# Kernel optimization log

Hardware: AMD Instinct MI355X
Metric: run time of the kernel (lower is better)

The kernel has to match this reference:

```python
import jax, jax.numpy as jnp
import numpy as np

N = 20000      # nodes
DEG = 16       # neighbors per destination node
E = N * DEG    # edges
G = 16         # graphs in batch


def _glorot(k, shape):
    lim = float(np.sqrt(6.0 / (shape[0] + shape[1])))
    return jax.random.uniform(k, shape, jnp.float32, -lim, lim)


def setup_inputs() -> dict:
    key = jax.random.key(0)
    ks = jax.random.split(key, 16)
    pos = jax.random.normal(ks[0], (N, 3), jnp.float32)
    edge_src = jax.random.randint(ks[1], (E,), 0, N)               # random neighbors
    edge_dst = jnp.repeat(jnp.arange(N), DEG)                       # every node is a dst
    batch = (jnp.arange(N) * G) // N                                # 16 contiguous graphs
    inp = {
        "pos": pos, "edge_src": edge_src, "edge_dst": edge_dst, "batch": batch,
        # conv1: mlp Linear(3+3 -> 128), Linear(128 -> 128)
        "c1_W1": _glorot(ks[2], (6, 128)),   "c1_b1": jnp.zeros((128,), jnp.float32),
        "c1_W2": _glorot(ks[3], (128, 128)), "c1_b2": jnp.zeros((128,), jnp.float32),
        # conv2: mlp Linear(128+3 -> 256), Linear(256 -> 256)
        "c2_W1": _glorot(ks[4], (131, 256)), "c2_b1": jnp.zeros((256,), jnp.float32),
        "c2_W2": _glorot(ks[5], (256, 256)), "c2_b2": jnp.zeros((256,), jnp.float32),
        "fc1_W": _glorot(ks[6], (256, 256)), "fc1_b": jnp.zeros((256,), jnp.float32),
        "fc2_W": _glorot(ks[7], (256, 128)), "fc2_b": jnp.zeros((128,), jnp.float32),
        "lab_W": _glorot(ks[8], (128, 10)),  "lab_b": jnp.zeros((10,), jnp.float32),
        "box_W": _glorot(ks[9], (128, 6)),   "box_b": jnp.zeros((6,), jnp.float32),
    }
    return inp


def _pointnet_conv(x, pos, src, dst, W1, b1, W2, b2):
    # gather: x_j, pos_j - pos_i per edge
    rel = pos[src] - pos[dst]                          # [E, 3]
    msg = jnp.concatenate([x[src], rel], axis=-1)      # [E, Cin+3]
    h = jnp.maximum(msg @ W1 + b1, 0.0) @ W2 + b2      # [E, Cout]
    # scatter-max aggregation per destination node (all nodes covered)
    return jax.ops.segment_max(h, dst, num_segments=N)


def reference(pos, edge_src, edge_dst, batch,
              c1_W1, c1_b1, c1_W2, c1_b2,
              c2_W1, c2_b1, c2_W2, c2_b2,
              fc1_W, fc1_b, fc2_W, fc2_b,
              lab_W, lab_b, box_W, box_b):
    x = pos  # model uses data.pos as both x and pos
    x = _pointnet_conv(x, pos, edge_src, edge_dst, c1_W1, c1_b1, c1_W2, c1_b2)
    x = _pointnet_conv(x, pos, edge_src, edge_dst, c2_W1, c2_b1, c2_W2, c2_b2)
    x = jax.ops.segment_max(x, batch, num_segments=G)  # global_max_pool -> [G, 256]
    x = jnp.maximum(x @ fc1_W + fc1_b, 0.0)
    x = jnp.maximum(x @ fc2_W + fc2_b, 0.0)
    labels = x @ lab_W + lab_b                          # [G, 10]
    bbox = x @ box_W + box_b                            # [G, 6]
    return (labels, bbox)
```

## Files before the change

kernel.cpp:

```cpp
#include <hip/hip_runtime.h>

#define N_NODES 20000
#define DEG 16
#define GRAPHS 16
#define NPG 1250

typedef __bf16 bf16x8 __attribute__((ext_vector_type(8)));
typedef float f32x4 __attribute__((ext_vector_type(4)));
#define MFMA16(a, b, c) __builtin_amdgcn_mfma_f32_16x16x32_bf16(a, b, c, 0, 0, 0)

__device__ __forceinline__ void ldsbar() {
    __asm__ volatile("s_waitcnt lgkmcnt(0)\n\ts_barrier" ::: "memory");
}
__device__ __forceinline__ void async16(void* lds, const void* g) {
    __builtin_amdgcn_global_load_lds(
        (const __attribute__((address_space(1))) unsigned int*)(g),
        (__attribute__((address_space(3))) unsigned int*)(lds), 16, 0, 0);
}

#define OFF_X1    0
#define OFF_P1    2560000
#define OFF_P2    2564096
#define OFF_P3    2580480
#define OFF_P4    2621440
#define OFF_POOL_BYTES 5373952
#define OFF_RELE  2695176
#define RELZ_ROW  320000
#define OFF_H1_BYTES 10510400

__global__ __launch_bounds__(256) void pack_weights(
    const float* __restrict__ c1W1, const float* __restrict__ c1W2,
    const float* __restrict__ c2W1, const float* __restrict__ c2W2,
    __bf16* __restrict__ p1, __bf16* __restrict__ p2,
    __bf16* __restrict__ p3, __bf16* __restrict__ p4,
    unsigned int* __restrict__ pooled, __bf16* __restrict__ relE)
{
    int t = blockIdx.x * 256 + threadIdx.x;
    if (t < GRAPHS * 256) pooled[t] = 0u;
    if (t == 0) {
        bf16x8 z;
        #pragma unroll
        for (int j = 0; j < 8; j++) z[j] = (__bf16)0.f;
        *(bf16x8*)&relE[(size_t)RELZ_ROW * 8] = z;
    }
    if (t >= 15872) return;
    const float* W; __bf16* out; int M, Kreal, KT, grp;
    if      (t <  512)  { W = c1W1; out = p1; M = 128; Kreal =   6; KT = 1; grp = t; }
    else if (t < 2560)  { W = c1W2; out = p2; M = 128; Kreal = 128; KT = 4; grp = t - 512; }
    else if (t < 7680)  { W = c2W1; out = p3; M = 256; Kreal = 131; KT = 5; grp = t - 2560; }
    else                { W = c2W2; out = p4; M = 256; Kreal = 256; KT = 8; grp = t - 7680; }
    int lane = grp & 63, rest = grp >> 6;
    int kt = rest % KT, mt = rest / KT;
    int m = mt * 16 + (lane & 15);
    int kbase = kt * 32 + ((lane >> 4) << 3);
    bf16x8 v;
    #pragma unroll
    for (int j = 0; j < 8; j++) {
        int k = kbase + j;
        v[j] = (k < Kreal) ? (__bf16)W[k * M + m] : (__bf16)0.f;
    }
    *(bf16x8*)&out[grp * 8] = v;
}

#define NB1 16
__global__ __launch_bounds__(256, 2) void conv1_kernel(
    const float* __restrict__ pos, const int* __restrict__ esrc,
    const __bf16* __restrict__ W1p, const float* __restrict__ b1,
    const __bf16* __restrict__ W2p, const float* __restrict__ b2,
    __bf16* __restrict__ x1, __bf16* __restrict__ relE)
{
    __shared__ __attribute__((aligned(16))) __bf16 msgF[NB1][16][8];
    __shared__ __attribute__((aligned(16))) __bf16 hidF[NB1 * 4 * 64 * 8];
    const int tid = threadIdx.x, lane = tid & 63, wave = tid >> 6;
    const int quad = lane >> 4, col = lane & 15;
    const int node0 = blockIdx.x * NB1;

    bf16x8 A1[2], B2w[2][4];
    f32x4 bias1[2];
    float b2v[2];
    #pragma unroll
    for (int i = 0; i < 2; i++) {
        int mtg = wave * 2 + i;
        A1[i] = *(const bf16x8*)&W1p[(mtg * 64 + lane) * 8];
        bias1[i] = *(const f32x4*)&b1[mtg * 16 + quad * 4];
        #pragma unroll
        for (int kt = 0; kt < 4; kt++)
            B2w[i][kt] = *(const bf16x8*)&W2p[((mtg * 4 + kt) * 64 + lane) * 8];
        b2v[i] = b2[mtg * 16 + col];
    }

    {
        int nl = tid >> 4, e = tid & 15;
        int d = node0 + nl;
        int s = esrc[d * 16 + e];
        float sx = pos[3*s], sy = pos[3*s+1], sz = pos[3*s+2];
        float dx = pos[3*d], dy = pos[3*d+1], dz = pos[3*d+2];
        __bf16 rx = (__bf16)(sx - dx), ry = (__bf16)(sy - dy), rz = (__bf16)(sz - dz);
        bf16x8 v;
        v[0] = (__bf16)sx; v[1] = (__bf16)sy; v[2] = (__bf16)sz;
        v[3] = rx; v[4] = ry; v[5] = rz;
        v[6] = (__bf16)0.f; v[7] = (__bf16)0.f;
        *(bf16x8*)&msgF[nl][e][0] = v;
        bf16x8 rv;
        rv[0] = rx; rv[1] = ry; rv[2] = rz;
        #pragma unroll
        for (int j = 3; j < 8; j++) rv[j] = (__bf16)0.f;
        *(bf16x8*)&relE[((size_t)d * 16 + e) * 8] = rv;
    }
    ldsbar();

    #pragma unroll
    for (int nl = 0; nl < NB1; nl++) {
        bf16x8 B;
        if (quad == 0) {
            B = *(const bf16x8*)&msgF[nl][col][0];
        } else {
            #pragma unroll
            for (int j = 0; j < 8; j++) B[j] = (__bf16)0.f;
        }
        #pragma unroll
        for (int i = 0; i < 2; i++) {
            int mtg = wave * 2 + i;
            f32x4 acc = bias1[i];
            acc = MFMA16(A1[i], B, acc);
            union { __bf16 h[4]; uint2 u; } pk;
            #pragma unroll
            for (int r = 0; r < 4; r++) pk.h[r] = (__bf16)fmaxf(acc[r], 0.f);
            int kt2 = mtg >> 1;
            int lane2 = ((mtg * 2 + (quad >> 1)) & 3) * 16 + col;
            int j0 = (quad & 1) * 4;
            *(uint2*)&hidF[((nl * 4 + kt2) * 64 + lane2) * 8 + j0] = pk.u;
        }
    }
    ldsbar();

    #pragma unroll
    for (int nl = 0; nl < NB1; nl++) {
        bf16x8 hA[4];
        #pragma unroll
        for (int kt = 0; kt < 4; kt++)
            hA[kt] = *(const bf16x8*)&hidF[((nl * 4 + kt) * 64 + lane) * 8];
        f32x4 acc[2];
        f32x4 z = {0.f, 0.f, 0.f, 0.f};
        acc[0] = z; acc[1] = z;
        #pragma unroll
        for (int kt = 0; kt < 4; kt++) {
            #pragma unroll
            for (int i = 0; i < 2; i++) acc[i] = MFMA16(hA[kt], B2w[i][kt], acc[i]);
        }
        #pragma unroll
        for (int i = 0; i < 2; i++) {
            int mtg = wave * 2 + i;
            float m = fmaxf(fmaxf(acc[i][0], acc[i][1]), fmaxf(acc[i][2], acc[i][3]));
            m = fmaxf(m, __shfl_xor(m, 16));
            m = fmaxf(m, __shfl_xor(m, 32));
            if (lane < 16)
                x1[(size_t)(node0 + nl) * 128 + mtg * 16 + lane] = (__bf16)(m + b2v[i]);
        }
    }
}

#define NB2 2
#define NT2 20
__global__ __launch_bounds__(512) __attribute__((amdgpu_waves_per_eu(2, 2)))
void conv2_kernel(
    const int* __restrict__ esrc,
    const __bf16* __restrict__ x1, const __bf16* __restrict__ relE,
    const __bf16* __restrict__ W1p, const float* __restrict__ b1,
    const __bf16* __restrict__ W2p, const float* __restrict__ b2,
    unsigned int* __restrict__ pooled)
{
    __shared__ __attribute__((aligned(16))) __bf16 msgF[3][NB2 * 5 * 64 * 8];
    __shared__ __attribute__((aligned(16))) __bf16 hidF[2][NB2 * 8 * 64 * 8];
    __shared__ int sSrc[NB2 * NT2 * 16];
    const int tid = threadIdx.x, lane = tid & 63, wave = tid >> 6;
    const int quad = lane >> 4, col = lane & 15;
    const int base = blockIdx.x * (NB2 * NT2);

    for (int u = tid; u < NB2 * NT2 * 16; u += 512) sSrc[u] = esrc[base * 16 + u];
    __syncthreads();

    if (wave < 4) {
        bf16x8 A1[4][5];
        f32x4 bias1[4];
        #pragma unroll
        for (int i = 0; i < 4; i++) {
            int tg = wave * 4 + i;
            #pragma unroll
            for (int kt = 0; kt < 5; kt++)
                A1[i][kt] = *(const bf16x8*)&W1p[((tg * 5 + kt) * 64 + lane) * 8];
            bias1[i] = *(const f32x4*)&b1[tg * 16 + quad * 4];
        }

        auto stage = [&](int td, int buf) {
            #pragma unroll
            for (int s = 0; s < 3; s++) {
                int g = wave + 4 * s;
                if (g < 10) {
                    int nl = g / 5, kt = g % 5;
                    __bf16* ldst = &msgF[buf][g * 64 * 8];
                    const __bf16* gsrc;
                    if (kt < 4) {
                        int src = sSrc[(td * NB2 + nl) * 16 + col];
                        gsrc = &x1[(size_t)src * 128 + kt * 32 + quad * 8];
                    } else {
                        int row = (quad == 0) ? ((base + td * NB2 + nl) * 16 + col) : RELZ_ROW;
                        gsrc = &relE[(size_t)row * 8];
                    }
                    async16(ldst, gsrc);
                }
            }
        };

        stage(0, 0);
        stage(1, 1);

        for (int k = 0; k < NT2; k++) {
            int td = k + 2;
            if (td >= NT2) td -= NT2;
            stage(td, (k + 2) % 3);
            if (wave < 2) __asm__ volatile("s_waitcnt vmcnt(6)" ::: "memory");
            else          __asm__ volatile("s_waitcnt vmcnt(4)" ::: "memory");
            const int bufi = k % 3, bufo = k & 1;
            #pragma unroll
            for (int nl = 0; nl < NB2; nl++) {
                bf16x8 B[5];
                #pragma unroll
                for (int kt = 0; kt < 5; kt++)
                    B[kt] = *(const bf16x8*)&msgF[bufi][((nl * 5 + kt) * 64 + lane) * 8];
                #pragma unroll
                for (int i = 0; i < 4; i++) {
                    int mtg = wave * 4 + i;
                    f32x4 acc = bias1[i];
                    #pragma unroll
                    for (int kt = 0; kt < 5; kt++) acc = MFMA16(A1[i][kt], B[kt], acc);
                    union { __bf16 h[4]; uint2 u; } pk;
                    #pragma unroll
                    for (int r = 0; r < 4; r++) pk.h[r] = (__bf16)fmaxf(acc[r], 0.f);
                    int kt2 = mtg >> 1;
                    int lane2 = ((mtg * 2 + (quad >> 1)) & 3) * 16 + col;
                    int j0 = (quad & 1) * 4;
                    *(uint2*)&hidF[bufo][((nl * 8 + kt2) * 64 + lane2) * 8 + j0] = pk.u;
                }
            }
            ldsbar();
        }
    } else {
        const int wv = wave - 4;
        bf16x8 B2r[4][8];
        #pragma unroll
        for (int i = 0; i < 4; i++) {
            int tg = wv * 4 + i;
            #pragma unroll
            for (int kt = 0; kt < 8; kt++)
                B2r[i][kt] = *(const bf16x8*)&W2p[((tg * 8 + kt) * 64 + lane) * 8];
        }
        f32x4 runmax[4];
        #pragma unroll
        for (int i = 0; i < 4; i++)
            #pragma unroll
            for (int r = 0; r < 4; r++) runmax[i][r] = -3.4e38f;
        int gprev = base / NPG;

        auto flushfn = [&]() {
            #pragma unroll
            for (int i = 0; i < 4; i++) {
                float v = fmaxf(fmaxf(runmax[i][0], runmax[i][1]),
                                fmaxf(runmax[i][2], runmax[i][3]));
                v = fmaxf(v, __shfl_xor(v, 16));
                v = fmaxf(v, __shfl_xor(v, 32));
                if (lane < 16) {
                    int c = (wv * 4 + i) * 16 + lane;
                    float val = v + b2[c];
                    unsigned u = __float_as_uint(val);
                    u = (u & 0x80000000u) ? ~u : (u | 0x80000000u);
                    atomicMax(&pooled[gprev * 256 + c], u);
                }
                #pragma unroll
                for (int r = 0; r < 4; r++) runmax[i][r] = -3.4e38f;
            }
        };
        auto consume = [&](int tk) {
            int buf1 = tk & 1;
            int n0 = base + tk * NB2;
            #pragma unroll
            for (int nl = 0; nl < NB2; nl++) {
                int g = (n0 + nl) / NPG;
                if (g != gprev) { flushfn(); gprev = g; }
                bf16x8 hA[8];
                #pragma unroll
                for (int kt = 0; kt < 8; kt++)
                    hA[kt] = *(const bf16x8*)&hidF[buf1][((nl * 8 + kt) * 64 + lane) * 8];
                f32x4 acc[4];
                f32x4 z = {0.f, 0.f, 0.f, 0.f};
                #pragma unroll
                for (int i = 0; i < 4; i++) acc[i] = z;
                #pragma unroll
                for (int kt = 0; kt < 8; kt++) {
                    #pragma unroll
                    for (int i = 0; i < 4; i++) acc[i] = MFMA16(hA[kt], B2r[i][kt], acc[i]);
                }
                #pragma unroll
                for (int i = 0; i < 4; i++)
                    #pragma unroll
                    for (int r = 0; r < 4; r++)
                        runmax[i][r] = fmaxf(runmax[i][r], acc[i][r]);
            }
        };

        for (int k = 0; k < NT2; k++) {
            ldsbar();
            consume(k);
        }
        flushfn();
    }
}

__global__ __launch_bounds__(256) void head1_kernel(
    const unsigned int* __restrict__ pooled,
    const float* __restrict__ fc1_W, const float* __restrict__ fc1_b,
    float* __restrict__ h1)
{
    __shared__ float p[256];
    const int g = blockIdx.x, c = threadIdx.x;
    unsigned u = pooled[g * 256 + c];
    u = (u & 0x80000000u) ? (u & 0x7fffffffu) : ~u;
    p[c] = __uint_as_float(u);
    __syncthreads();
    float acc = fc1_b[c];
    #pragma unroll 8
    for (int k = 0; k < 256; k++) acc += p[k] * fc1_W[k * 256 + c];
    h1[g * 256 + c] = fmaxf(acc, 0.f);
}

__global__ __launch_bounds__(128) void head2_kernel(
    const float* __restrict__ h1,
    const float* __restrict__ fc2_W, const float* __restrict__ fc2_b,
    const float* __restrict__ lab_W, const float* __restrict__ lab_b,
    const float* __restrict__ box_W, const float* __restrict__ box_b,
    float* __restrict__ out)
{
    __shared__ float hs[256];
    __shared__ float h2s[128];
    const int g = blockIdx.x, c = threadIdx.x;
    hs[c]       = h1[g * 256 + c];
    hs[c + 128] = h1[g * 256 + 128 + c];
    __syncthreads();
    float acc = fc2_b[c];
    #pragma unroll 8
    for (int k = 0; k < 256; k++) acc += hs[k] * fc2_W[k * 128 + c];
    h2s[c] = fmaxf(acc, 0.f);
    __syncthreads();
    if (c < 10) {
        float a = lab_b[c];
        #pragma unroll 8
        for (int k = 0; k < 128; k++) a += h2s[k] * lab_W[k * 10 + c];
        out[g * 10 + c] = a;
    } else if (c < 16) {
        int j = c - 10;
        float a = box_b[j];
        #pragma unroll 8
        for (int k = 0; k < 128; k++) a += h2s[k] * box_W[k * 6 + j];
        out[160 + g * 6 + j] = a;
    }
}

extern "C" void kernel_launch(void* const* d_in, const int* in_sizes, int n_in,
                              void* d_out, int out_size, void* d_ws, size_t ws_size,
                              hipStream_t stream) {
    const float* pos   = (const float*)d_in[0];
    const int*   esrc  = (const int*)  d_in[1];
    const float* c1W1 = (const float*)d_in[4];
    const float* c1b1 = (const float*)d_in[5];
    const float* c1W2 = (const float*)d_in[6];
    const float* c1b2 = (const float*)d_in[7];
    const float* c2W1 = (const float*)d_in[8];
    const float* c2b1 = (const float*)d_in[9];
    const float* c2W2 = (const float*)d_in[10];
    const float* c2b2 = (const float*)d_in[11];
    const float* fc1W = (const float*)d_in[12];
    const float* fc1b = (const float*)d_in[13];
    const float* fc2W = (const float*)d_in[14];
    const float* fc2b = (const float*)d_in[15];
    const float* labW = (const float*)d_in[16];
    const float* labb = (const float*)d_in[17];
    const float* boxW = (const float*)d_in[18];
    const float* boxb = (const float*)d_in[19];

    __bf16* wsb = (__bf16*)d_ws;
    __bf16* x1   = wsb + OFF_X1;
    __bf16* p1   = wsb + OFF_P1;
    __bf16* p2   = wsb + OFF_P2;
    __bf16* p3   = wsb + OFF_P3;
    __bf16* p4   = wsb + OFF_P4;
    __bf16* relE = wsb + OFF_RELE;
    unsigned int* pooled = (unsigned int*)((char*)d_ws + OFF_POOL_BYTES);
    float* h1 = (float*)((char*)d_ws + OFF_H1_BYTES);

    pack_weights<<<62, 256, 0, stream>>>(c1W1, c1W2, c2W1, c2W2, p1, p2, p3, p4, pooled, relE);
    conv1_kernel<<<N_NODES / NB1, 256, 0, stream>>>(pos, esrc, p1, c1b1, p2, c1b2, x1, relE);
    conv2_kernel<<<N_NODES / (NB2 * NT2), 512, 0, stream>>>(esrc, x1, relE, p3, c2b1, p4, c2b2, pooled);
    head1_kernel<<<GRAPHS, 256, 0, stream>>>(pooled, fc1W, fc1b, h1);
    head2_kernel<<<GRAPHS, 128, 0, stream>>>(h1, fc2W, fc2b, labW, labb, boxW, boxb, (float*)d_out);
}
```

Before: 215.6 us.

## Split edge gather into own kernel, warp-specialize conv1, fuse head kernels

Edge message construction (source position plus relative position) now runs in a separate gather kernel that writes a full 8-wide bf16 message per edge. Conv2's packed first-layer weights are remapped so its rel slot reads from columns 3-5 of that message. Conv1 becomes a producer/consumer kernel: four waves async-load messages into triple-buffered LDS and run layer 1, while four waves run layer 2 and the max reduction from double-buffered hidden tiles. The two head kernels are merged into one 1024-thread kernel with split-K reductions, which removes a launch and the h1 round trip. The cost is an extra launch and a global write and read of per-edge messages.

```diff
diff --git a/kernel.cpp b/kernel.cpp
--- a/kernel.cpp
+++ b/kernel.cpp
@@ -24,16 +24,15 @@
 #define OFF_P3    2580480
 #define OFF_P4    2621440
 #define OFF_POOL_BYTES 5373952
-#define OFF_RELE  2695176
-#define RELZ_ROW  320000
-#define OFF_H1_BYTES 10510400
+#define OFF_MSGE  2695176
+#define ZROW      320000
 
 __global__ __launch_bounds__(256) void pack_weights(
     const float* __restrict__ c1W1, const float* __restrict__ c1W2,
     const float* __restrict__ c2W1, const float* __restrict__ c2W2,
     __bf16* __restrict__ p1, __bf16* __restrict__ p2,
     __bf16* __restrict__ p3, __bf16* __restrict__ p4,
-    unsigned int* __restrict__ pooled, __bf16* __restrict__ relE)
+    unsigned int* __restrict__ pooled, __bf16* __restrict__ msgE)
 {
     int t = blockIdx.x * 256 + threadIdx.x;
     if (t < GRAPHS * 256) pooled[t] = 0u;
@@ -41,13 +40,13 @@
         bf16x8 z;
         #pragma unroll
         for (int j = 0; j < 8; j++) z[j] = (__bf16)0.f;
-        *(bf16x8*)&relE[(size_t)RELZ_ROW * 8] = z;
+        *(bf16x8*)&msgE[(size_t)ZROW * 8] = z;
     }
     if (t >= 15872) return;
-    const float* W; __bf16* out; int M, Kreal, KT, grp;
+    const float* W; __bf16* out; int M, Kreal, KT, grp; bool c2w1 = false;
     if      (t <  512)  { W = c1W1; out = p1; M = 128; Kreal =   6; KT = 1; grp = t; }
     else if (t < 2560)  { W = c1W2; out = p2; M = 128; Kreal = 128; KT = 4; grp = t - 512; }
-    else if (t < 7680)  { W = c2W1; out = p3; M = 256; Kreal = 131; KT = 5; grp = t - 2560; }
+    else if (t < 7680)  { W = c2W1; out = p3; M = 256; Kreal = 131; KT = 5; grp = t - 2560; c2w1 = true; }
     else                { W = c2W2; out = p4; M = 256; Kreal = 256; KT = 8; grp = t - 7680; }
     int lane = grp & 63, rest = grp >> 6;
     int kt = rest % KT, mt = rest / KT;
@@ -56,106 +55,125 @@
     bf16x8 v;
     #pragma unroll
     for (int j = 0; j < 8; j++) {
-        int k = kbase + j;
-        v[j] = (k < Kreal) ? (__bf16)W[k * M + m] : (__bf16)0.f;
+        int ks = kbase + j;
+        int wr;
+        if (c2w1) wr = (ks < 128) ? ks : ((ks >= 131 && ks < 134) ? ks - 3 : -1);
+        else      wr = (ks < Kreal) ? ks : -1;
+        v[j] = (wr >= 0) ? (__bf16)W[wr * M + m] : (__bf16)0.f;
     }
     *(bf16x8*)&out[grp * 8] = v;
 }
 
-#define NB1 16
-__global__ __launch_bounds__(256, 2) void conv1_kernel(
+__global__ __launch_bounds__(256) void gatherE_kernel(
     const float* __restrict__ pos, const int* __restrict__ esrc,
+    __bf16* __restrict__ msgE)
+{
+    int e = blockIdx.x * 256 + threadIdx.x;
+    int d = e >> 4;
+    int s = esrc[e];
+    float sx = pos[3*s], sy = pos[3*s+1], sz = pos[3*s+2];
+    float dx = pos[3*d], dy = pos[3*d+1], dz = pos[3*d+2];
+    bf16x8 v;
+    v[0] = (__bf16)sx; v[1] = (__bf16)sy; v[2] = (__bf16)sz;
+    v[3] = (__bf16)(sx - dx); v[4] = (__bf16)(sy - dy); v[5] = (__bf16)(sz - dz);
+    v[6] = (__bf16)0.f; v[7] = (__bf16)0.f;
+    *(bf16x8*)&msgE[(size_t)e * 8] = v;
+}
+
+#define NB1T 4
+#define NT1 10
+__global__ __launch_bounds__(512, 4) void conv1_kernel(
+    const __bf16* __restrict__ msgE,
     const __bf16* __restrict__ W1p, const float* __restrict__ b1,
     const __bf16* __restrict__ W2p, const float* __restrict__ b2,
-    __bf16* __restrict__ x1, __bf16* __restrict__ relE)
+    __bf16* __restrict__ x1)
 {
-    __shared__ __attribute__((aligned(16))) __bf16 msgF[NB1][16][8];
-    __shared__ __attribute__((aligned(16))) __bf16 hidF[NB1 * 4 * 64 * 8];
+    __shared__ __attribute__((aligned(16))) __bf16 msgF[3][NB1T * 64 * 8];
+    __shared__ __attribute__((aligned(16))) __bf16 hidF[2][NB1T * 4 * 64 * 8];
     const int tid = threadIdx.x, lane = tid & 63, wave = tid >> 6;
     const int quad = lane >> 4, col = lane & 15;
-    const int node0 = blockIdx.x * NB1;
-
-    bf16x8 A1[2], B2w[2][4];
-    f32x4 bias1[2];
-    float b2v[2];
-    #pragma unroll
-    for (int i = 0; i < 2; i++) {
-        int mtg = wave * 2 + i;
-        A1[i] = *(const bf16x8*)&W1p[(mtg * 64 + lane) * 8];
-        bias1[i] = *(const f32x4*)&b1[mtg * 16 + quad * 4];
-        #pragma unroll
-        for (int kt = 0; kt < 4; kt++)
-            B2w[i][kt] = *(const bf16x8*)&W2p[((mtg * 4 + kt) * 64 + lane) * 8];
-        b2v[i] = b2[mtg * 16 + col];
-    }
-
-    {
-        int nl = tid >> 4, e = tid & 15;
-        int d = node0 + nl;
-        int s = esrc[d * 16 + e];
-        float sx = pos[3*s], sy = pos[3*s+1], sz = pos[3*s+2];
-        float dx = pos[3*d], dy = pos[3*d+1], dz = pos[3*d+2];
-        __bf16 rx = (__bf16)(sx - dx), ry = (__bf16)(sy - dy), rz = (__bf16)(sz - dz);
-        bf16x8 v;
-        v[0] = (__bf16)sx; v[1] = (__bf16)sy; v[2] = (__bf16)sz;
-        v[3] = rx; v[4] = ry; v[5] = rz;
-        v[6] = (__bf16)0.f; v[7] = (__bf16)0.f;
-        *(bf16x8*)&msgF[nl][e][0] = v;
-        bf16x8 rv;
-        rv[0] = rx; rv[1] = ry; rv[2] = rz;
-        #pragma unroll
-        for (int j = 3; j < 8; j++) rv[j] = (__bf16)0.f;
-        *(bf16x8*)&relE[((size_t)d * 16 + e) * 8] = rv;
-    }
-    ldsbar();
-
-    #pragma unroll
-    for (int nl = 0; nl < NB1; nl++) {
-        bf16x8 B;
-        if (quad == 0) {
-            B = *(const bf16x8*)&msgF[nl][col][0];
-        } else {
-            #pragma unroll
-            for (int j = 0; j < 8; j++) B[j] = (__bf16)0.f;
-        }
+    const int base = blockIdx.x * (NB1T * NT1);
+
+    if (wave < 4) {
+        bf16x8 A1[2];
+        f32x4 bias1[2];
         #pragma unroll
         for (int i = 0; i < 2; i++) {
             int mtg = wave * 2 + i;
-            f32x4 acc = bias1[i];
-            acc = MFMA16(A1[i], B, acc);
-            union { __bf16 h[4]; uint2 u; } pk;
-            #pragma unroll
-            for (int r = 0; r < 4; r++) pk.h[r] = (__bf16)fmaxf(acc[r], 0.f);
-            int kt2 = mtg >> 1;
-            int lane2 = ((mtg * 2 + (quad >> 1)) & 3) * 16 + col;
-            int j0 = (quad & 1) * 4;
-            *(uint2*)&hidF[((nl * 4 + kt2) * 64 + lane2) * 8 + j0] = pk.u;
-        }
-    }
-    ldsbar();
-
-    #pragma unroll
-    for (int nl = 0; nl < NB1; nl++) {
-        bf16x8 hA[4];
-        #pragma unroll
-        for (int kt = 0; kt < 4; kt++)
-            hA[kt] = *(const bf16x8*)&hidF[((nl * 4 + kt) * 64 + lane) * 8];
-        f32x4 acc[2];
-        f32x4 z = {0.f, 0.f, 0.f, 0.f};
-        acc[0] = z; acc[1] = z;
-        #pragma unroll
-        for (int kt = 0; kt < 4; kt++) {
-            #pragma unroll
-            for (int i = 0; i < 2; i++) acc[i] = MFMA16(hA[kt], B2w[i][kt], acc[i]);
-        }
+            A1[i] = *(const bf16x8*)&W1p[(mtg * 64 + lane) * 8];
+            bias1[i] = *(const f32x4*)&b1[mtg * 16 + quad * 4];
+        }
+        auto stage = [&](int td, int buf) {
+            int nl = wave;
+            int row = (quad == 0) ? ((base + td * NB1T + nl) * 16 + col) : ZROW;
+            async16(&msgF[buf][nl * 64 * 8], &msgE[(size_t)row * 8]);
+        };
+        stage(0, 0);
+        stage(1, 1);
+        for (int k = 0; k < NT1; k++) {
+            int td = k + 2; if (td >= NT1) td -= NT1;
+            stage(td, (k + 2) % 3);
+            __asm__ volatile("s_waitcnt vmcnt(2)" ::: "memory");
+            const int bufi = k % 3, bufo = k & 1;
+            #pragma unroll
+            for (int nl = 0; nl < NB1T; nl++) {
+                bf16x8 B = *(const bf16x8*)&msgF[bufi][(nl * 64 + lane) * 8];
+                #pragma unroll
+                for (int i = 0; i < 2; i++) {
+                    int mtg = wave * 2 + i;
+                    f32x4 acc = bias1[i];
+                    acc = MFMA16(A1[i], B, acc);
+                    union { __bf16 h[4]; uint2 u; } pk;
+                    #pragma unroll
+                    for (int r = 0; r < 4; r++) pk.h[r] = (__bf16)fmaxf(acc[r], 0.f);
+                    int kt2 = mtg >> 1;
+                    int lane2 = ((mtg * 2 + (quad >> 1)) & 3) * 16 + col;
+                    int j0 = (quad & 1) * 4;
+                    *(uint2*)&hidF[bufo][((nl * 4 + kt2) * 64 + lane2) * 8 + j0] = pk.u;
+                }
+            }
+            ldsbar();
+        }
+    } else {
+        const int wv = wave - 4;
+        bf16x8 B2w[2][4];
+        float b2v[2];
         #pragma unroll
         for (int i = 0; i < 2; i++) {
-            int mtg = wave * 2 + i;
-            float m = fmaxf(fmaxf(acc[i][0], acc[i][1]), fmaxf(acc[i][2], acc[i][3]));
-            m = fmaxf(m, __shfl_xor(m, 16));
-            m = fmaxf(m, __shfl_xor(m, 32));
-            if (lane < 16)
-                x1[(size_t)(node0 + nl) * 128 + mtg * 16 + lane] = (__bf16)(m + b2v[i]);
+            int mtg = wv * 2 + i;
+            #pragma unroll
+            for (int kt = 0; kt < 4; kt++)
+                B2w[i][kt] = *(const bf16x8*)&W2p[((mtg * 4 + kt) * 64 + lane) * 8];
+            b2v[i] = b2[mtg * 16 + col];
+        }
+        for (int k = 0; k < NT1; k++) {
+            ldsbar();
+            const int buf = k & 1;
+            const int n0 = base + k * NB1T;
+            #pragma unroll
+            for (int nl = 0; nl < NB1T; nl++) {
+                bf16x8 hA[4];
+                #pragma unroll
+                for (int kt = 0; kt < 4; kt++)
+                    hA[kt] = *(const bf16x8*)&hidF[buf][((nl * 4 + kt) * 64 + lane) * 8];
+                f32x4 acc[2];
+                f32x4 z = {0.f, 0.f, 0.f, 0.f};
+                acc[0] = z; acc[1] = z;
+                #pragma unroll
+                for (int kt = 0; kt < 4; kt++) {
+                    #pragma unroll
+                    for (int i = 0; i < 2; i++) acc[i] = MFMA16(hA[kt], B2w[i][kt], acc[i]);
+                }
+                #pragma unroll
+                for (int i = 0; i < 2; i++) {
+                    float m = fmaxf(fmaxf(acc[i][0], acc[i][1]), fmaxf(acc[i][2], acc[i][3]));
+                    m = fmaxf(m, __shfl_xor(m, 16));
+                    m = fmaxf(m, __shfl_xor(m, 32));
+                    if (lane < 16)
+                        x1[(size_t)(n0 + nl) * 128 + (wv * 2 + i) * 16 + lane] =
+                            (__bf16)(m + b2v[i]);
+                }
+            }
         }
     }
 }
@@ -165,7 +183,7 @@
 __global__ __launch_bounds__(512) __attribute__((amdgpu_waves_per_eu(2, 2)))
 void conv2_kernel(
     const int* __restrict__ esrc,
-    const __bf16* __restrict__ x1, const __bf16* __restrict__ relE,
+    const __bf16* __restrict__ x1, const __bf16* __restrict__ msgE,
     const __bf16* __restrict__ W1p, const float* __restrict__ b1,
     const __bf16* __restrict__ W2p, const float* __restrict__ b2,
     unsigned int* __restrict__ pooled)
@@ -204,8 +222,8 @@
                         int src = sSrc[(td * NB2 + nl) * 16 + col];
                         gsrc = &x1[(size_t)src * 128 + kt * 32 + quad * 8];
                     } else {
-                        int row = (quad == 0) ? ((base + td * NB2 + nl) * 16 + col) : RELZ_ROW;
-                        gsrc = &relE[(size_t)row * 8];
+                        int row = (quad == 0) ? ((base + td * NB2 + nl) * 16 + col) : ZROW;
+                        gsrc = &msgE[(size_t)row * 8];
                     }
                     async16(ldst, gsrc);
                 }
@@ -316,52 +334,70 @@
     }
 }
 
-__global__ __launch_bounds__(256) void head1_kernel(
+__global__ __launch_bounds__(1024) void head_kernel(
     const unsigned int* __restrict__ pooled,
     const float* __restrict__ fc1_W, const float* __restrict__ fc1_b,
-    float* __restrict__ h1)
-{
-    __shared__ float p[256];
-    const int g = blockIdx.x, c = threadIdx.x;
-    unsigned u = pooled[g * 256 + c];
-    u = (u & 0x80000000u) ? (u & 0x7fffffffu) : ~u;
-    p[c] = __uint_as_float(u);
-    __syncthreads();
-    float acc = fc1_b[c];
-    #pragma unroll 8
-    for (int k = 0; k < 256; k++) acc += p[k] * fc1_W[k * 256 + c];
-    h1[g * 256 + c] = fmaxf(acc, 0.f);
-}
-
-__global__ __launch_bounds__(128) void head2_kernel(
-    const float* __restrict__ h1,
     const float* __restrict__ fc2_W, const float* __restrict__ fc2_b,
     const float* __restrict__ lab_W, const float* __restrict__ lab_b,
     const float* __restrict__ box_W, const float* __restrict__ box_b,
     float* __restrict__ out)
 {
-    __shared__ float hs[256];
-    __shared__ float h2s[128];
-    const int g = blockIdx.x, c = threadIdx.x;
-    hs[c]       = h1[g * 256 + c];
-    hs[c + 128] = h1[g * 256 + 128 + c];
-    __syncthreads();
-    float acc = fc2_b[c];
-    #pragma unroll 8
-    for (int k = 0; k < 256; k++) acc += hs[k] * fc2_W[k * 128 + c];
-    h2s[c] = fmaxf(acc, 0.f);
-    __syncthreads();
-    if (c < 10) {
-        float a = lab_b[c];
+    __shared__ float p[256], h1s[256], h2s[128], red[1024];
+    const int g = blockIdx.x, tid = threadIdx.x;
+    if (tid < 256) {
+        unsigned u = pooled[g * 256 + tid];
+        u = (u & 0x80000000u) ? (u & 0x7fffffffu) : ~u;
+        p[tid] = __uint_as_float(u);
+    }
+    __syncthreads();
+    {
+        int c = tid & 255, kq = tid >> 8;
+        float a = 0.f;
         #pragma unroll 8
-        for (int k = 0; k < 128; k++) a += h2s[k] * lab_W[k * 10 + c];
-        out[g * 10 + c] = a;
-    } else if (c < 16) {
-        int j = c - 10;
-        float a = box_b[j];
+        for (int k0 = 0; k0 < 64; k0++) {
+            int k = kq * 64 + k0;
+            a += p[k] * fc1_W[k * 256 + c];
+        }
+        red[tid] = a;
+    }
+    __syncthreads();
+    if (tid < 256)
+        h1s[tid] = fmaxf(red[tid] + red[256 + tid] + red[512 + tid] + red[768 + tid]
+                         + fc1_b[tid], 0.f);
+    __syncthreads();
+    if (tid < 512) {
+        int c = tid & 127, kq = tid >> 7;
+        float a = 0.f;
         #pragma unroll 8
-        for (int k = 0; k < 128; k++) a += h2s[k] * box_W[k * 6 + j];
-        out[160 + g * 6 + j] = a;
+        for (int k0 = 0; k0 < 64; k0++) {
+            int k = kq * 64 + k0;
+            a += h1s[k] * fc2_W[k * 128 + c];
+        }
+        red[tid] = a;
+    }
+    __syncthreads();
+    if (tid < 128)
+        h2s[tid] = fmaxf(red[tid] + red[128 + tid] + red[256 + tid] + red[384 + tid]
+                         + fc2_b[tid], 0.f);
+    __syncthreads();
+    if (tid < 128) {
+        int o = tid >> 3, kq = tid & 7;
+        float a = 0.f;
+        #pragma unroll
+        for (int k0 = 0; k0 < 16; k0++) {
+            int k = kq * 16 + k0;
+            float w = (o < 10) ? lab_W[k * 10 + o] : box_W[k * 6 + (o - 10)];
+            a += h2s[k] * w;
+        }
+        red[tid] = a;
+    }
+    __syncthreads();
+    if (tid < 16) {
+        float a = 0.f;
+        #pragma unroll
+        for (int q = 0; q < 8; q++) a += red[tid * 8 + q];
+        if (tid < 10) out[g * 10 + tid] = a + lab_b[tid];
+        else          out[160 + g * 6 + (tid - 10)] = a + box_b[tid - 10];
     }
 }
 
@@ -393,13 +429,13 @@
     __bf16* p2   = wsb + OFF_P2;
     __bf16* p3   = wsb + OFF_P3;
     __bf16* p4   = wsb + OFF_P4;
-    __bf16* relE = wsb + OFF_RELE;
+    __bf16* msgE = wsb + OFF_MSGE;
     unsigned int* pooled = (unsigned int*)((char*)d_ws + OFF_POOL_BYTES);
-    float* h1 = (float*)((char*)d_ws + OFF_H1_BYTES);
-
-    pack_weights<<<62, 256, 0, stream>>>(c1W1, c1W2, c2W1, c2W2, p1, p2, p3, p4, pooled, relE);
-    conv1_kernel<<<N_NODES / NB1, 256, 0, stream>>>(pos, esrc, p1, c1b1, p2, c1b2, x1, relE);
-    conv2_kernel<<<N_NODES / (NB2 * NT2), 512, 0, stream>>>(esrc, x1, relE, p3, c2b1, p4, c2b2, pooled);
-    head1_kernel<<<GRAPHS, 256, 0, stream>>>(pooled, fc1W, fc1b, h1);
-    head2_kernel<<<GRAPHS, 128, 0, stream>>>(h1, fc2W, fc2b, labW, labb, boxW, boxb, (float*)d_out);
-}
+
+    pack_weights<<<62, 256, 0, stream>>>(c1W1, c1W2, c2W1, c2W2, p1, p2, p3, p4, pooled, msgE);
+    gatherE_kernel<<<1250, 256, 0, stream>>>(pos, esrc, msgE);
+    conv1_kernel<<<N_NODES / (NB1T * NT1), 512, 0, stream>>>(msgE, p1, c1b1, p2, c1b2, x1);
+    conv2_kernel<<<N_NODES / (NB2 * NT2), 512, 0, stream>>>(esrc, x1, msgE, p3, c2b1, p4, c2b2, pooled);
+    head_kernel<<<GRAPHS, 1024, 0, stream>>>(pooled, fc1W, fc1b, fc2W, fc2b,
+                                             labW, labb, boxW, boxb, (float*)d_out);
+}
```

Result: faster. 192.4 us (-10.8%).
